# Kernel optimization log

Hardware: AMD Instinct MI355X
Metric: run time of the kernel (lower is better)

## Reference

```python
import jax, jax.numpy as jnp
import numpy as np

DIM, DEPTH, HEADS, DHEAD, FF = 768, 6, 12, 64, 3072


def layer_norm(x, g, b, eps=1e-5):
    m = jnp.mean(x, axis=-1, keepdims=True)
    v = jnp.mean((x - m) ** 2, axis=-1, keepdims=True)
    return (x - m) * jax.lax.rsqrt(v + eps) * g + b


def setup_inputs() -> dict:
    key = jax.random.key(0)
    ks = jax.random.split(key, 8)
    s = 0.02
    inp = {
        "x": jax.random.normal(ks[0], (2, 2048, DIM), jnp.float32),
        "mask": jnp.ones((2, 2048), dtype=bool),
        "ln1_g": jnp.ones((DEPTH, DIM)), "ln1_b": jnp.zeros((DEPTH, DIM)),
        "w_qkv": jax.random.normal(ks[1], (DEPTH, DIM, 3 * HEADS * DHEAD)) * s,
        "w_out": jax.random.normal(ks[2], (DEPTH, HEADS * DHEAD, DIM)) * s,
        "b_out": jnp.zeros((DEPTH, DIM)),
        "ln2_g": jnp.ones((DEPTH, DIM)), "ln2_b": jnp.zeros((DEPTH, DIM)),
        "w_ff1": jax.random.normal(ks[3], (DEPTH, DIM, FF)) * s,
        "b_ff1": jnp.zeros((DEPTH, FF)),
        "w_ff2": jax.random.normal(ks[4], (DEPTH, FF, DIM)) * s,
        "b_ff2": jnp.zeros((DEPTH, DIM)),
        "lnf_g": jnp.ones((DIM,)), "lnf_b": jnp.zeros((DIM,)),
    }
    return inp


def reference(x, mask, ln1_g, ln1_b, w_qkv, w_out, b_out, ln2_g, ln2_b,
              w_ff1, b_ff1, w_ff2, b_ff2, lnf_g, lnf_b):
    scale = DHEAD ** -0.5
    b, n, _ = x.shape
    neg = -jnp.finfo(x.dtype).max
    mask4 = mask[:, None, None, :]  # b 1 1 j
    for l in range(DEPTH):
        # --- attention (pre-norm) ---
        h = layer_norm(x, ln1_g[l], ln1_b[l])
        qkv = h @ w_qkv[l]                           # [b, n, 3*h*d]
        q, k, v = jnp.split(qkv, 3, axis=-1)
        q = q.reshape(b, n, HEADS, DHEAD).transpose(0, 2, 1, 3)
        k = k.reshape(b, n, HEADS, DHEAD).transpose(0, 2, 1, 3)
        v = v.reshape(b, n, HEADS, DHEAD).transpose(0, 2, 1, 3)
        sim = jnp.einsum('bhid,bhjd->bhij', q, k) * scale
        sim = jnp.where(mask4, sim, neg)
        attn = jax.nn.softmax(sim, axis=-1)
        o = jnp.einsum('bhij,bhjd->bhid', attn, v)
        o = o.transpose(0, 2, 1, 3).reshape(b, n, HEADS * DHEAD)
        x = o @ w_out[l] + b_out[l] + x
        # --- feedforward (pre-norm) ---
        h = layer_norm(x, ln2_g[l], ln2_b[l])
        h = jax.nn.gelu(h @ w_ff1[l] + b_ff1[l], approximate=False)
        x = h @ w_ff2[l] + b_ff2[l] + x
    return layer_norm(x, lnf_g, lnf_b)
```

## Files before the change

kernel.cpp:

```cpp
#include <hip/hip_runtime.h>
#include <hip/hip_bf16.h>

typedef __attribute__((ext_vector_type(8))) short bf16x8;
typedef __attribute__((ext_vector_type(4))) float f32x4;
typedef __attribute__((ext_vector_type(16))) float f32x16;

#define DIMM 768
#define SEQ 2048
#define NBATCH 2
#define MTOT 4096
#define NHEAD 12
#define FFD 3072
#define NZ 2

static __device__ __forceinline__ unsigned short f2bfbits(float f) {
  __hip_bfloat16 h = __float2bfloat16(f);
  return __builtin_bit_cast(unsigned short, h);
}
static __device__ __forceinline__ float bf2f(short u) {
  unsigned bits = ((unsigned)(unsigned short)u) << 16;
  return __builtin_bit_cast(float, bits);
}
static __device__ __forceinline__ unsigned packbf2(float lo, float hi) {
  return (unsigned)f2bfbits(lo) | ((unsigned)f2bfbits(hi) << 16);
}
static __device__ __forceinline__ float fexp2(float x) {
  float r; asm("v_exp_f32 %0, %1" : "=v"(r) : "v"(x)); return r;
}

__global__ __launch_bounds__(256) void wconv_all(const float* __restrict__ wq,
                                                 const float* __restrict__ wo,
                                                 const float* __restrict__ wf1,
                                                 const float* __restrict__ wf2,
                                                 __hip_bfloat16* __restrict__ oq,
                                                 __hip_bfloat16* __restrict__ oo,
                                                 __hip_bfloat16* __restrict__ of1,
                                                 __hip_bfloat16* __restrict__ of2) {
  __shared__ float tile[32][33];
  int id = blockIdx.x;
  const float* in; __hip_bfloat16* out; int R, C;
  if (id < 1728)      { in = wq;  out = oq;  R = 768;  C = 2304; }
  else if (id < 2304) { id -= 1728; in = wo;  out = oo;  R = 768;  C = 768; }
  else if (id < 4608) { id -= 2304; in = wf1; out = of1; R = 768;  C = 3072; }
  else                { id -= 4608; in = wf2; out = of2; R = 3072; C = 768; }
  int tc = C >> 5;
  int rb = (id / tc) * 32, cb = (id % tc) * 32;
  int t = threadIdx.x;
  int r = t >> 3, c4 = (t & 7) << 2;
  float4 v = *(const float4*)(in + (size_t)(rb + r) * C + cb + c4);
  tile[r][c4] = v.x; tile[r][c4 + 1] = v.y; tile[r][c4 + 2] = v.z; tile[r][c4 + 3] = v.w;
  __syncthreads();
  ushort4 u;
  u.x = f2bfbits(tile[c4][r]);
  u.y = f2bfbits(tile[c4 + 1][r]);
  u.z = f2bfbits(tile[c4 + 2][r]);
  u.w = f2bfbits(tile[c4 + 3][r]);
  *(ushort4*)((unsigned short*)out + (size_t)(cb + r) * R + rb + c4) = u;
}

template<bool OUT_BF16>
__global__ __launch_bounds__(192) void ln_kernel(const float* __restrict__ x,
                                                 const float* __restrict__ g,
                                                 const float* __restrict__ b,
                                                 void* __restrict__ out) {
  int row = blockIdx.x;
  int tid = threadIdx.x;
  const float* xr = x + (size_t)row * DIMM;
  float4 v = *(const float4*)(xr + tid * 4);
  float s = v.x + v.y + v.z + v.w;
  float s2 = v.x * v.x + v.y * v.y + v.z * v.z + v.w * v.w;
  #pragma unroll
  for (int off = 32; off >= 1; off >>= 1) {
    s += __shfl_xor(s, off);
    s2 += __shfl_xor(s2, off);
  }
  __shared__ float red[6];
  int wv = tid >> 6;
  if ((tid & 63) == 0) { red[wv] = s; red[3 + wv] = s2; }
  __syncthreads();
  s = red[0] + red[1] + red[2];
  s2 = red[3] + red[4] + red[5];
  float mean = s * (1.f / DIMM);
  float var = fmaxf(s2 * (1.f / DIMM) - mean * mean, 0.f);
  float rs = rsqrtf(var + 1e-5f);
  float4 gv = *(const float4*)(g + tid * 4);
  float4 bv = *(const float4*)(b + tid * 4);
  float o0 = (v.x - mean) * rs * gv.x + bv.x;
  float o1 = (v.y - mean) * rs * gv.y + bv.y;
  float o2 = (v.z - mean) * rs * gv.z + bv.z;
  float o3 = (v.w - mean) * rs * gv.w + bv.w;
  if (OUT_BF16) {
    ushort4 u;
    u.x = f2bfbits(o0); u.y = f2bfbits(o1); u.z = f2bfbits(o2); u.w = f2bfbits(o3);
    *(ushort4*)((unsigned short*)out + (size_t)row * DIMM + tid * 4) = u;
  } else {
    float4 o;
    o.x = o0; o.y = o1; o.z = o2; o.w = o3;
    *(float4*)((float*)out + (size_t)row * DIMM + tid * 4) = o;
  }
}

enum { EPI_BF16 = 0, EPI_GELU_BF16 = 1, EPI_RES_F32 = 2, EPI_QKV = 3 };

template<int EPI, int BM, int BN, int BK>
__global__ __launch_bounds__(256) void gemm_nt(const __hip_bfloat16* __restrict__ A,
                                               const __hip_bfloat16* __restrict__ Bt,
                                               const float* __restrict__ bias,
                                               const float* resid,
                                               void* Cout, __hip_bfloat16* vtout,
                                               int M, int N, int K) {
  constexpr int FM = BM / 32, FN = BN / 32;
  constexpr int NKB = BK / 32;
  constexpr int CPR = BK / 8;
  constexpr int RPL = 512 / BK;
  constexpr int TLA = BM * BK / 512, TLB = BN * BK / 512;
  __shared__ __hip_bfloat16 Alds[2][BM * BK];
  __shared__ __hip_bfloat16 Blds[2][BN * BK];
  const int tid = threadIdx.x;
  const int lane = tid & 63, wid = tid >> 6;
  const int wm = wid >> 1, wn = wid & 1;
  const int lo = lane & 15, hi = lane >> 4;
  const int m0 = blockIdx.x * BM, n0 = blockIdx.y * BN;
  const int lrow = lane / CPR;
  const int lcc = lane % CPR;

  auto stage = [&](int buf, int k0) {
    #pragma unroll
    for (int c = 0; c < (TLA + 3) / 4; ++c) {
      int ld = c * 4 + wid;
      if (TLA % 4 == 0 || ld < TLA) {
        int row = ld * RPL + lrow;
        int cc = lcc ^ (row & (CPR - 1));
        const __hip_bfloat16* ga = A + (size_t)(m0 + row) * K + k0 + cc * 8;
        __builtin_amdgcn_global_load_lds((const __attribute__((address_space(1))) void*)ga,
                                         (__attribute__((address_space(3))) void*)(&Alds[buf][0] + ld * 512), 16, 0, 0);
      }
    }
    #pragma unroll
    for (int c = 0; c < (TLB + 3) / 4; ++c) {
      int ld = c * 4 + wid;
      if (TLB % 4 == 0 || ld < TLB) {
        int row = ld * RPL + lrow;
        int cc = lcc ^ (row & (CPR - 1));
        const __hip_bfloat16* gb = Bt + (size_t)(n0 + row) * K + k0 + cc * 8;
        __builtin_amdgcn_global_load_lds((const __attribute__((address_space(1))) void*)gb,
                                         (__attribute__((address_space(3))) void*)(&Blds[buf][0] + ld * 512), 16, 0, 0);
      }
    }
  };

  f32x4 acc[FM][FN] = {};
  stage(0, 0);
  __syncthreads();
  int cur = 0;
  for (int k0 = 0; k0 < K; k0 += BK) {
    if (k0 + BK < K) stage(cur ^ 1, k0 + BK);
    const __hip_bfloat16* Ab = &Alds[cur][0];
    const __hip_bfloat16* Bb = &Blds[cur][0];
    bf16x8 af[FM][NKB], bfr[FN][NKB];
    #pragma unroll
    for (int m = 0; m < FM; ++m) {
      int row = wm * (BM / 2) + m * 16 + lo;
      #pragma unroll
      for (int s = 0; s < NKB; ++s)
        af[m][s] = *(const bf16x8*)(Ab + row * BK + 8 * ((s * 4 + hi) ^ (row & (CPR - 1))));
    }
    #pragma unroll
    for (int n = 0; n < FN; ++n) {
      int row = wn * (BN / 2) + n * 16 + lo;
      #pragma unroll
      for (int s = 0; s < NKB; ++s)
        bfr[n][s] = *(const bf16x8*)(Bb + row * BK + 8 * ((s * 4 + hi) ^ (row & (CPR - 1))));
    }
    #pragma unroll
    for (int s = 0; s < NKB; ++s)
      #pragma unroll
      for (int m = 0; m < FM; ++m)
        #pragma unroll
        for (int n = 0; n < FN; ++n)
          acc[m][n] = __builtin_amdgcn_mfma_f32_16x16x32_bf16(af[m][s], bfr[n][s], acc[m][n], 0, 0, 0);
    __syncthreads();
    cur ^= 1;
  }
  if (EPI == EPI_QKV && n0 >= 1536) {
    #pragma unroll
    for (int m = 0; m < FM; ++m) {
      int rowb = m0 + wm * (BM / 2) + m * 16 + hi * 4;
      int b = rowb >> 11, q = rowb & 2047;
      #pragma unroll
      for (int n = 0; n < FN; ++n) {
        int col = n0 + wn * (BN / 2) + n * 16 + lo;
        int dg = col - 1536;
        int hh = dg >> 6, d = dg & 63;
        ushort4 u;
        u.x = f2bfbits(acc[m][n][0]);
        u.y = f2bfbits(acc[m][n][1]);
        u.z = f2bfbits(acc[m][n][2]);
        u.w = f2bfbits(acc[m][n][3]);
        *(ushort4*)((unsigned short*)vtout + (((size_t)(b * NHEAD + hh) * 64 + d) << 11) + q) = u;
      }
    }
    return;
  }
  #pragma unroll
  for (int m = 0; m < FM; ++m) {
    int rowb = m0 + wm * (BM / 2) + m * 16 + hi * 4;
    #pragma unroll
    for (int n = 0; n < FN; ++n) {
      int col = n0 + wn * (BN / 2) + n * 16 + lo;
      float bv = (EPI == EPI_BF16 || EPI == EPI_QKV) ? 0.f : bias[col];
      #pragma unroll
      for (int i = 0; i < 4; ++i) {
        float v = acc[m][n][i] + bv;
        size_t idx = (size_t)(rowb + i) * N + col;
        if (EPI == EPI_GELU_BF16) {
          v = 0.5f * v * (1.f + erff(v * 0.70710678118654752f));
          ((unsigned short*)Cout)[idx] = f2bfbits(v);
        } else if (EPI == EPI_RES_F32) {
          ((float*)Cout)[idx] = v + resid[idx];
        } else {
          ((unsigned short*)Cout)[idx] = f2bfbits(v);
        }
      }
    }
  }
}

__global__ __launch_bounds__(256) void attn_kernel(const __hip_bfloat16* __restrict__ qkv,
                                                   const __hip_bfloat16* __restrict__ vt,
                                                   __hip_bfloat16* __restrict__ opart,
                                                   float2* __restrict__ mlbuf) {
  __shared__ __hip_bfloat16 Klds[2][64 * 64];
  __shared__ __hip_bfloat16 Vlds[2][64 * 64];
  const int tid = threadIdx.x;
  const int lane = tid & 63, wid = tid >> 6;
  const int q32 = lane & 31, h5 = lane >> 5;
  const int bh = blockIdx.y, bb = bh / NHEAD, h = bh % NHEAD;
  const int z = blockIdx.z;
  const int kvbase = z * (SEQ / NZ);
  const int q0 = blockIdx.x * 128 + wid * 32;
  const size_t pitch = 3 * DIMM;

  bf16x8 qf[4];
  {
    const __hip_bfloat16* Qp = qkv + (size_t)(bb * SEQ + q0 + q32) * pitch + h * 64;
    #pragma unroll
    for (int t4 = 0; t4 < 4; ++t4) {
      bf16x8 r = *(const bf16x8*)(Qp + t4 * 16 + h5 * 8);
      #pragma unroll
      for (int j = 0; j < 8; ++j)
        r[j] = (short)f2bfbits(bf2f(r[j]) * 0.18033688011112042f);
      qf[t4] = r;
    }
  }

  const int sk = tid >> 2;
  const int sc = tid & 3;
  const __hip_bfloat16* Kg = qkv + (size_t)bb * SEQ * pitch + DIMM + h * 64;
  const __hip_bfloat16* Vg = vt + (size_t)bh * 64 * SEQ;
  const int kswz0 = 8 * (sc ^ (sk & 7));
  const int kswz1 = 8 * ((sc + 4) ^ (sk & 7));

  bf16x8 k0r, k1r, v0r, v1r;
  {
    const __hip_bfloat16* kg = Kg + (size_t)(kvbase + sk) * pitch;
    k0r = *(const bf16x8*)(kg + sc * 8);
    k1r = *(const bf16x8*)(kg + sc * 8 + 32);
    const __hip_bfloat16* vg = Vg + (size_t)sk * SEQ + kvbase;
    v0r = *(const bf16x8*)(vg + sc * 8);
    v1r = *(const bf16x8*)(vg + sc * 8 + 32);
  }

  f32x16 accO0 = {}, accO1 = {};
  float m_run = -1e30f, l_run = 0.f;

  const int NT = (SEQ / NZ) / 64;
  for (int t = 0; t < NT; ++t) {
    __hip_bfloat16* Kb = Klds[t & 1];
    __hip_bfloat16* Vb = Vlds[t & 1];
    *(bf16x8*)(Kb + sk * 64 + kswz0) = k0r;
    *(bf16x8*)(Kb + sk * 64 + kswz1) = k1r;
    *(bf16x8*)(Vb + sk * 64 + kswz0) = v0r;
    *(bf16x8*)(Vb + sk * 64 + kswz1) = v1r;
    __syncthreads();
    if (t + 1 < NT) {
      int kv0 = kvbase + (t + 1) * 64;
      const __hip_bfloat16* kg = Kg + (size_t)(kv0 + sk) * pitch;
      k0r = *(const bf16x8*)(kg + sc * 8);
      k1r = *(const bf16x8*)(kg + sc * 8 + 32);
      const __hip_bfloat16* vg = Vg + (size_t)sk * SEQ + kv0;
      v0r = *(const bf16x8*)(vg + sc * 8);
      v1r = *(const bf16x8*)(vg + sc * 8 + 32);
    }

    #pragma unroll
    for (int sub = 0; sub < 2; ++sub) {
      const int krow = sub * 32 + q32;
      f32x16 sacc = {};
      __builtin_amdgcn_s_setprio(1);
      #pragma unroll
      for (int t4 = 0; t4 < 4; ++t4) {
        bf16x8 kf = *(const bf16x8*)(Kb + krow * 64 + 8 * ((2 * t4 + h5) ^ (krow & 7)));
        sacc = __builtin_amdgcn_mfma_f32_32x32x16_bf16(kf, qf[t4], sacc, 0, 0, 0);
      }
      __builtin_amdgcn_s_setprio(0);
      float t0 = fmaxf(fmaxf(sacc[0], sacc[1]), sacc[2]);
      float t1 = fmaxf(fmaxf(sacc[3], sacc[4]), sacc[5]);
      float t2 = fmaxf(fmaxf(sacc[6], sacc[7]), sacc[8]);
      float t3 = fmaxf(fmaxf(sacc[9], sacc[10]), sacc[11]);
      float t4m = fmaxf(fmaxf(sacc[12], sacc[13]), sacc[14]);
      float vmax = fmaxf(fmaxf(fmaxf(t0, t1), t2), fmaxf(fmaxf(t3, t4m), sacc[15]));
      vmax = fmaxf(vmax, __shfl_xor(vmax, 32));
      if (!__all(vmax <= m_run + 8.f)) {
        float mnew = fmaxf(m_run, vmax);
        float alpha = fexp2(m_run - mnew);
        #pragma unroll
        for (int r = 0; r < 16; ++r) { accO0[r] *= alpha; accO1[r] *= alpha; }
        l_run *= alpha;
        m_run = mnew;
      }
      float p[16];
      #pragma unroll
      for (int r = 0; r < 16; ++r) p[r] = fexp2(sacc[r] - m_run);
      float sr[8];
      #pragma unroll
      for (int r = 0; r < 8; ++r) sr[r] = p[r] + p[r + 8];
      #pragma unroll
      for (int r = 0; r < 4; ++r) sr[r] = sr[r] + sr[r + 4];
      float lsum = (sr[0] + sr[1]) + (sr[2] + sr[3]);
      lsum += __shfl_xor(lsum, 32);
      l_run += lsum;
      unsigned c0 = packbf2(p[0], p[1]),   c1 = packbf2(p[2], p[3]);
      unsigned c2 = packbf2(p[4], p[5]),   c3 = packbf2(p[6], p[7]);
      unsigned c4 = packbf2(p[8], p[9]),   c5 = packbf2(p[10], p[11]);
      unsigned c6 = packbf2(p[12], p[13]), c7 = packbf2(p[14], p[15]);
      auto r20 = __builtin_amdgcn_permlane32_swap((int)c2, (int)c0, false, false);
      auto r31 = __builtin_amdgcn_permlane32_swap((int)c3, (int)c1, false, false);
      auto r64 = __builtin_amdgcn_permlane32_swap((int)c6, (int)c4, false, false);
      auto r75 = __builtin_amdgcn_permlane32_swap((int)c7, (int)c5, false, false);
      int4 pw0i = { r20[1], r31[1], r20[0], r31[0] };
      int4 pw1i = { r64[1], r75[1], r64[0], r75[0] };
      bf16x8 pf0 = __builtin_bit_cast(bf16x8, pw0i);
      bf16x8 pf1 = __builtin_bit_cast(bf16x8, pw1i);
      const int d0 = q32, d1 = 32 + q32;
      bf16x8 a00 = *(const bf16x8*)(Vb + d0 * 64 + 8 * ((sub * 4 + 0 + h5) ^ (d0 & 7)));
      bf16x8 a01 = *(const bf16x8*)(Vb + d0 * 64 + 8 * ((sub * 4 + 2 + h5) ^ (d0 & 7)));
      bf16x8 a10 = *(const bf16x8*)(Vb + d1 * 64 + 8 * ((sub * 4 + 0 + h5) ^ (d1 & 7)));
      bf16x8 a11 = *(const bf16x8*)(Vb + d1 * 64 + 8 * ((sub * 4 + 2 + h5) ^ (d1 & 7)));
      __builtin_amdgcn_s_setprio(1);
      accO0 = __builtin_amdgcn_mfma_f32_32x32x16_bf16(a00, pf0, accO0, 0, 0, 0);
      accO0 = __builtin_amdgcn_mfma_f32_32x32x16_bf16(a01, pf1, accO0, 0, 0, 0);
      accO1 = __builtin_amdgcn_mfma_f32_32x32x16_bf16(a10, pf0, accO1, 0, 0, 0);
      accO1 = __builtin_amdgcn_mfma_f32_32x32x16_bf16(a11, pf1, accO1, 0, 0, 0);
      __builtin_amdgcn_s_setprio(0);
    }
  }

  float linv = 1.f / l_run;
  unsigned short* orow = (unsigned short*)opart + (size_t)z * MTOT * DIMM +
                         (size_t)(bb * SEQ + q0 + q32) * DIMM + h * 64;
  #pragma unroll
  for (int g = 0; g < 4; ++g) {
    ushort4 u0, u1;
    u0.x = f2bfbits(accO0[g * 4 + 0] * linv);
    u0.y = f2bfbits(accO0[g * 4 + 1] * linv);
    u0.z = f2bfbits(accO0[g * 4 + 2] * linv);
    u0.w = f2bfbits(accO0[g * 4 + 3] * linv);
    *(ushort4*)(orow + g * 8 + h5 * 4) = u0;
    u1.x = f2bfbits(accO1[g * 4 + 0] * linv);
    u1.y = f2bfbits(accO1[g * 4 + 1] * linv);
    u1.z = f2bfbits(accO1[g * 4 + 2] * linv);
    u1.w = f2bfbits(accO1[g * 4 + 3] * linv);
    *(ushort4*)(orow + 32 + g * 8 + h5 * 4) = u1;
  }
  if (h5 == 0)
    mlbuf[((size_t)(z * 24 + bh) << 11) + q0 + q32] = make_float2(m_run, l_run);
}

__global__ __launch_bounds__(256) void attn_combine(const __hip_bfloat16* __restrict__ opart,
                                                    const float2* __restrict__ ml,
                                                    __hip_bfloat16* __restrict__ out) {
  int g = blockIdx.x * 256 + threadIdx.x;
  int row = g / 96;
  int cw = g - row * 96;
  int h = cw >> 3;
  int b = row >> 11, q = row & 2047;
  int bh = b * NHEAD + h;
  float2 mlz[NZ];
  #pragma unroll
  for (int z = 0; z < NZ; ++z)
    mlz[z] = ml[((size_t)(z * 24 + bh) << 11) + q];
  float m = mlz[0].x;
  #pragma unroll
  for (int z = 1; z < NZ; ++z) m = fmaxf(m, mlz[z].x);
  float w[NZ], wsum = 0.f;
  #pragma unroll
  for (int z = 0; z < NZ; ++z) { w[z] = fexp2(mlz[z].x - m) * mlz[z].y; wsum += w[z]; }
  float inv = 1.f / wsum;
  size_t off = (size_t)row * DIMM + cw * 8;
  float accv[8] = {};
  #pragma unroll
  for (int z = 0; z < NZ; ++z) {
    bf16x8 o = *(const bf16x8*)((const unsigned short*)opart + (size_t)z * MTOT * DIMM + off);
    float wz = w[z] * inv;
    #pragma unroll
    for (int j = 0; j < 8; ++j) accv[j] += wz * bf2f(o[j]);
  }
  bf16x8 r;
  #pragma unroll
  for (int j = 0; j < 8; ++j) r[j] = (short)f2bfbits(accv[j]);
  *(bf16x8*)((unsigned short*)out + off) = r;
}

extern "C" void kernel_launch(void* const* d_in, const int* in_sizes, int n_in,
                              void* d_out, int out_size, void* d_ws, size_t ws_size,
                              hipStream_t stream) {
  const float* x_in  = (const float*)d_in[0];
  const float* ln1_g = (const float*)d_in[2];
  const float* ln1_b = (const float*)d_in[3];
  const float* w_qkv = (const float*)d_in[4];
  const float* w_out = (const float*)d_in[5];
  const float* b_out = (const float*)d_in[6];
  const float* ln2_g = (const float*)d_in[7];
  const float* ln2_b = (const float*)d_in[8];
  const float* w_ff1 = (const float*)d_in[9];
  const float* b_ff1 = (const float*)d_in[10];
  const float* w_ff2 = (const float*)d_in[11];
  const float* b_ff2 = (const float*)d_in[12];
  const float* lnf_g = (const float*)d_in[13];
  const float* lnf_b = (const float*)d_in[14];

  const size_t OFF_X    = 0;
  const size_t OFF_H    = 12582912;
  const size_t OFF_QKV  = OFF_H + 6291456;
  const size_t OFF_AO   = OFF_QKV + 18874368;
  const size_t OFF_FFH  = OFF_AO + 6291456;
  const size_t OFF_WQKV = OFF_FFH + 25165824;
  const size_t OFF_WOUT = OFF_WQKV + 3538944;
  const size_t OFF_WFF1 = OFF_WOUT + 1179648;
  const size_t OFF_WFF2 = OFF_WFF1 + 4718592;
  const size_t NEED     = OFF_WFF2 + 4718592;
  if (ws_size < NEED) return;

  char* ws = (char*)d_ws;
  float* x              = (float*)(ws + OFF_X);
  __hip_bfloat16* h     = (__hip_bfloat16*)(ws + OFF_H);
  float2* mlbuf         = (float2*)(ws + OFF_H);
  __hip_bfloat16* qkvb  = (__hip_bfloat16*)(ws + OFF_QKV);
  __hip_bfloat16* ao    = (__hip_bfloat16*)(ws + OFF_AO);
  __hip_bfloat16* vtb   = (__hip_bfloat16*)(ws + OFF_AO);
  __hip_bfloat16* ffh   = (__hip_bfloat16*)(ws + OFF_FFH);
  __hip_bfloat16* opart = (__hip_bfloat16*)(ws + OFF_FFH);
  __hip_bfloat16* wqkvt = (__hip_bfloat16*)(ws + OFF_WQKV);
  __hip_bfloat16* woutt = (__hip_bfloat16*)(ws + OFF_WOUT);
  __hip_bfloat16* wff1t = (__hip_bfloat16*)(ws + OFF_WFF1);
  __hip_bfloat16* wff2t = (__hip_bfloat16*)(ws + OFF_WFF2);

  hipMemcpyAsync(x, x_in, (size_t)MTOT * DIMM * 4, hipMemcpyDeviceToDevice, stream);

  for (int l = 0; l < 6; ++l) {
    wconv_all<<<6912, 256, 0, stream>>>(
        w_qkv + (size_t)l * DIMM * 3 * DIMM,
        w_out + (size_t)l * DIMM * DIMM,
        w_ff1 + (size_t)l * DIMM * FFD,
        w_ff2 + (size_t)l * FFD * DIMM,
        wqkvt, woutt, wff1t, wff2t);

    ln_kernel<true><<<MTOT, 192, 0, stream>>>(x, ln1_g + l * DIMM, ln1_b + l * DIMM, h);
    gemm_nt<EPI_QKV, 128, 96, 32><<<dim3(MTOT / 128, (3 * DIMM) / 96), 256, 0, stream>>>(
        h, wqkvt, nullptr, nullptr, qkvb, vtb, MTOT, 3 * DIMM, DIMM);
    attn_kernel<<<dim3(SEQ / 128, NBATCH * NHEAD, NZ), 256, 0, stream>>>(qkvb, vtb, opart, mlbuf);
    attn_combine<<<(MTOT * DIMM / 8) / 256, 256, 0, stream>>>(opart, mlbuf, ao);
    gemm_nt<EPI_RES_F32, 64, 64, 64><<<dim3(MTOT / 64, DIMM / 64), 256, 0, stream>>>(
        ao, woutt, b_out + l * DIMM, x, x, nullptr, MTOT, DIMM, DIMM);
    ln_kernel<true><<<MTOT, 192, 0, stream>>>(x, ln2_g + l * DIMM, ln2_b + l * DIMM, h);
    gemm_nt<EPI_GELU_BF16, 128, 96, 32><<<dim3(MTOT / 128, FFD / 96), 256, 0, stream>>>(
        h, wff1t, b_ff1 + (size_t)l * FFD, nullptr, ffh, nullptr, MTOT, FFD, DIMM);
    gemm_nt<EPI_RES_F32, 64, 64, 64><<<dim3(MTOT / 64, DIMM / 64), 256, 0, stream>>>(
        ffh, wff2t, b_ff2 + l * DIMM, x, x, nullptr, MTOT, DIMM, FFD);
  }
  ln_kernel<false><<<MTOT, 192, 0, stream>>>(x, lnf_g, lnf_b, d_out);
}
```

Measured before the change: 1.095 ms.

## Fuse fp32 weight conversion and transpose into GEMM B-tile staging

Drops the separate per-layer weight conversion kernel that transposed fp32 weights to bf16 in workspace. The GEMM now reads fp32 weights directly, converts them to bf16 and writes the transposed tiles into LDS with synchronous per-thread loads. This removes one launch and one write-plus-reread of about 14M weight elements per layer. In exchange, every M-block now re-reads and re-converts the fp32 weights, and B staging loses the async global-to-LDS path, so it can no longer overlap with compute the same way.

```diff
diff --git a/kernel.cpp b/kernel.cpp
--- a/kernel.cpp
+++ b/kernel.cpp
@@ -26,36 +26,6 @@
 }
 static __device__ __forceinline__ float fexp2(float x) {
   float r; asm("v_exp_f32 %0, %1" : "=v"(r) : "v"(x)); return r;
-}
-
-__global__ __launch_bounds__(256) void wconv_all(const float* __restrict__ wq,
-                                                 const float* __restrict__ wo,
-                                                 const float* __restrict__ wf1,
-                                                 const float* __restrict__ wf2,
-                                                 __hip_bfloat16* __restrict__ oq,
-                                                 __hip_bfloat16* __restrict__ oo,
-                                                 __hip_bfloat16* __restrict__ of1,
-                                                 __hip_bfloat16* __restrict__ of2) {
-  __shared__ float tile[32][33];
-  int id = blockIdx.x;
-  const float* in; __hip_bfloat16* out; int R, C;
-  if (id < 1728)      { in = wq;  out = oq;  R = 768;  C = 2304; }
-  else if (id < 2304) { id -= 1728; in = wo;  out = oo;  R = 768;  C = 768; }
-  else if (id < 4608) { id -= 2304; in = wf1; out = of1; R = 768;  C = 3072; }
-  else                { id -= 4608; in = wf2; out = of2; R = 3072; C = 768; }
-  int tc = C >> 5;
-  int rb = (id / tc) * 32, cb = (id % tc) * 32;
-  int t = threadIdx.x;
-  int r = t >> 3, c4 = (t & 7) << 2;
-  float4 v = *(const float4*)(in + (size_t)(rb + r) * C + cb + c4);
-  tile[r][c4] = v.x; tile[r][c4 + 1] = v.y; tile[r][c4 + 2] = v.z; tile[r][c4 + 3] = v.w;
-  __syncthreads();
-  ushort4 u;
-  u.x = f2bfbits(tile[c4][r]);
-  u.y = f2bfbits(tile[c4 + 1][r]);
-  u.z = f2bfbits(tile[c4 + 2][r]);
-  u.w = f2bfbits(tile[c4 + 3][r]);
-  *(ushort4*)((unsigned short*)out + (size_t)(cb + r) * R + rb + c4) = u;
 }
 
 template<bool OUT_BF16>
@@ -104,7 +74,7 @@
 
 template<int EPI, int BM, int BN, int BK>
 __global__ __launch_bounds__(256) void gemm_nt(const __hip_bfloat16* __restrict__ A,
-                                               const __hip_bfloat16* __restrict__ Bt,
+                                               const float* __restrict__ Wsrc,
                                                const float* __restrict__ bias,
                                                const float* resid,
                                                void* Cout, __hip_bfloat16* vtout,
@@ -113,7 +83,8 @@
   constexpr int NKB = BK / 32;
   constexpr int CPR = BK / 8;
   constexpr int RPL = 512 / BK;
-  constexpr int TLA = BM * BK / 512, TLB = BN * BK / 512;
+  constexpr int TLA = BM * BK / 512;
+  constexpr int BITEMS = BN * (BK / 8);
   __shared__ __hip_bfloat16 Alds[2][BM * BK];
   __shared__ __hip_bfloat16 Blds[2][BN * BK];
   const int tid = threadIdx.x;
@@ -124,7 +95,7 @@
   const int lrow = lane / CPR;
   const int lcc = lane % CPR;
 
-  auto stage = [&](int buf, int k0) {
+  auto stageA = [&](int buf, int k0) {
     #pragma unroll
     for (int c = 0; c < (TLA + 3) / 4; ++c) {
       int ld = c * 4 + wid;
@@ -136,25 +107,34 @@
                                          (__attribute__((address_space(3))) void*)(&Alds[buf][0] + ld * 512), 16, 0, 0);
       }
     }
-    #pragma unroll
-    for (int c = 0; c < (TLB + 3) / 4; ++c) {
-      int ld = c * 4 + wid;
-      if (TLB % 4 == 0 || ld < TLB) {
-        int row = ld * RPL + lrow;
-        int cc = lcc ^ (row & (CPR - 1));
-        const __hip_bfloat16* gb = Bt + (size_t)(n0 + row) * K + k0 + cc * 8;
-        __builtin_amdgcn_global_load_lds((const __attribute__((address_space(1))) void*)gb,
-                                         (__attribute__((address_space(3))) void*)(&Blds[buf][0] + ld * 512), 16, 0, 0);
-      }
-    }
   };
+  auto stageB = [&](int buf, int k0) {
+    #pragma unroll
+    for (int it0 = 0; it0 < BITEMS; it0 += 256) {
+      int it = it0 + tid;
+      if (BITEMS % 256 == 0 || it < BITEMS) {
+        int n = it % BN;
+        int c = it / BN;
+        const float* gs = Wsrc + (size_t)(k0 + c * 8) * N + n0 + n;
+        unsigned short u[8];
+        #pragma unroll
+        for (int j = 0; j < 8; ++j) u[j] = f2bfbits(gs[(size_t)j * N]);
+        int cs = c ^ (n & (CPR - 1));
+        *(bf16x8*)(&Blds[buf][0] + n * BK + cs * 8) = *(const bf16x8*)u;
+      }
+    }
+  };
 
   f32x4 acc[FM][FN] = {};
-  stage(0, 0);
+  stageA(0, 0);
+  stageB(0, 0);
   __syncthreads();
   int cur = 0;
   for (int k0 = 0; k0 < K; k0 += BK) {
-    if (k0 + BK < K) stage(cur ^ 1, k0 + BK);
+    if (k0 + BK < K) {
+      stageA(cur ^ 1, k0 + BK);
+      stageB(cur ^ 1, k0 + BK);
+    }
     const __hip_bfloat16* Ab = &Alds[cur][0];
     const __hip_bfloat16* Bb = &Blds[cur][0];
     bf16x8 af[FM][NKB], bfr[FN][NKB];
@@ -435,11 +415,7 @@
   const size_t OFF_QKV  = OFF_H + 6291456;
   const size_t OFF_AO   = OFF_QKV + 18874368;
   const size_t OFF_FFH  = OFF_AO + 6291456;
-  const size_t OFF_WQKV = OFF_FFH + 25165824;
-  const size_t OFF_WOUT = OFF_WQKV + 3538944;
-  const size_t OFF_WFF1 = OFF_WOUT + 1179648;
-  const size_t OFF_WFF2 = OFF_WFF1 + 4718592;
-  const size_t NEED     = OFF_WFF2 + 4718592;
+  const size_t NEED     = OFF_FFH + 25165824;
   if (ws_size < NEED) return;
 
   char* ws = (char*)d_ws;
@@ -451,33 +427,27 @@
   __hip_bfloat16* vtb   = (__hip_bfloat16*)(ws + OFF_AO);
   __hip_bfloat16* ffh   = (__hip_bfloat16*)(ws + OFF_FFH);
   __hip_bfloat16* opart = (__hip_bfloat16*)(ws + OFF_FFH);
-  __hip_bfloat16* wqkvt = (__hip_bfloat16*)(ws + OFF_WQKV);
-  __hip_bfloat16* woutt = (__hip_bfloat16*)(ws + OFF_WOUT);
-  __hip_bfloat16* wff1t = (__hip_bfloat16*)(ws + OFF_WFF1);
-  __hip_bfloat16* wff2t = (__hip_bfloat16*)(ws + OFF_WFF2);
 
   hipMemcpyAsync(x, x_in, (size_t)MTOT * DIMM * 4, hipMemcpyDeviceToDevice, stream);
 
   for (int l = 0; l < 6; ++l) {
-    wconv_all<<<6912, 256, 0, stream>>>(
-        w_qkv + (size_t)l * DIMM * 3 * DIMM,
-        w_out + (size_t)l * DIMM * DIMM,
-        w_ff1 + (size_t)l * DIMM * FFD,
-        w_ff2 + (size_t)l * FFD * DIMM,
-        wqkvt, woutt, wff1t, wff2t);
+    const float* wq  = w_qkv + (size_t)l * DIMM * 3 * DIMM;
+    const float* wo  = w_out + (size_t)l * DIMM * DIMM;
+    const float* wf1 = w_ff1 + (size_t)l * DIMM * FFD;
+    const float* wf2 = w_ff2 + (size_t)l * FFD * DIMM;
 
     ln_kernel<true><<<MTOT, 192, 0, stream>>>(x, ln1_g + l * DIMM, ln1_b + l * DIMM, h);
     gemm_nt<EPI_QKV, 128, 96, 32><<<dim3(MTOT / 128, (3 * DIMM) / 96), 256, 0, stream>>>(
-        h, wqkvt, nullptr, nullptr, qkvb, vtb, MTOT, 3 * DIMM, DIMM);
+        h, wq, nullptr, nullptr, qkvb, vtb, MTOT, 3 * DIMM, DIMM);
     attn_kernel<<<dim3(SEQ / 128, NBATCH * NHEAD, NZ), 256, 0, stream>>>(qkvb, vtb, opart, mlbuf);
     attn_combine<<<(MTOT * DIMM / 8) / 256, 256, 0, stream>>>(opart, mlbuf, ao);
     gemm_nt<EPI_RES_F32, 64, 64, 64><<<dim3(MTOT / 64, DIMM / 64), 256, 0, stream>>>(
-        ao, woutt, b_out + l * DIMM, x, x, nullptr, MTOT, DIMM, DIMM);
+        ao, wo, b_out + l * DIMM, x, x, nullptr, MTOT, DIMM, DIMM);
     ln_kernel<true><<<MTOT, 192, 0, stream>>>(x, ln2_g + l * DIMM, ln2_b + l * DIMM, h);
     gemm_nt<EPI_GELU_BF16, 128, 96, 32><<<dim3(MTOT / 128, FFD / 96), 256, 0, stream>>>(
-        h, wff1t, b_ff1 + (size_t)l * FFD, nullptr, ffh, nullptr, MTOT, FFD, DIMM);
+        h, wf1, b_ff1 + (size_t)l * FFD, nullptr, ffh, nullptr, MTOT, FFD, DIMM);
     gemm_nt<EPI_RES_F32, 64, 64, 64><<<dim3(MTOT / 64, DIMM / 64), 256, 0, stream>>>(
-        ffh, wff2t, b_ff2 + l * DIMM, x, x, nullptr, MTOT, DIMM, FFD);
+        ffh, wf2, b_ff2 + l * DIMM, x, x, nullptr, MTOT, DIMM, FFD);
   }
   ln_kernel<false><<<MTOT, 192, 0, stream>>>(x, lnf_g, lnf_b, d_out);
 }
```

Result: slower. 1.302 ms (+18.9%).
